# Optimization experiments

Measured on AMD Instinct MI355X. Metric: run time of the kernel, lower is better.

Reference implementation:

```python
import jax, jax.numpy as jnp
import numpy as np

N = 10000
E = 320000
D = 256   # hidden_dim
H = 4     # heads
C = D // H
NL = 3    # gat layers
EPS = 1e-5


def _ln(x, g, b):
    m = x.mean(-1, keepdims=True)
    v = ((x - m) ** 2).mean(-1, keepdims=True)
    return (x - m) / jnp.sqrt(v + EPS) * g + b


def setup_inputs() -> dict:
    key = jax.random.key(0)
    ks = iter(jax.random.split(key, 64))
    rn = lambda shape, s=0.05: jax.random.normal(next(ks), shape, dtype=jnp.float32) * s
    inp = dict(
        x=jax.random.normal(next(ks), (N, 10), dtype=jnp.float32),
        edge_index=jax.random.randint(next(ks), (2, E), 0, N),
        edge_attr=jax.random.uniform(next(ks), (E, 3), dtype=jnp.float32),
        agent_features=jax.random.normal(next(ks), (1, 10), dtype=jnp.float32),
        # node encoder
        enc_w=rn((10, D)), enc_b=jnp.zeros(D), enc_g=jnp.ones(D), enc_bt=jnp.zeros(D),
        # adaptive virtual node
        vn_base=jnp.zeros(D), vn_w1=rn((D, D)), vn_b1=jnp.zeros(D),
        vn_g=jnp.ones(D), vn_bt=jnp.zeros(D), vn_w2=rn((D, D)), vn_b2=jnp.zeros(D),
        # stacked GAT layer params
        gat_w=rn((NL, D, D)), att_src=rn((NL, H, C)), att_dst=rn((NL, H, C)),
        att_edge=rn((NL, H, C)), edge_w=rn((NL, 3, D)), gat_b=jnp.zeros((NL, D)),
        ln_g=jnp.ones((NL, D)), ln_b=jnp.zeros((NL, D)),
        # agent encoder
        ag_w=rn((10, D)), ag_b=jnp.zeros(D), ag_g=jnp.ones(D), ag_bt=jnp.zeros(D),
        # dueling heads (jk_dim = D*(NL+1) + D)
        v_w1=rn((D * (NL + 2), D)), v_b1=jnp.zeros(D), v_g=jnp.ones(D), v_bt=jnp.zeros(D),
        v_w2=rn((D, 1)), v_b2=jnp.zeros(1),
        a_w1=rn((D * (NL + 2), D)), a_b1=jnp.zeros(D), a_g=jnp.ones(D), a_bt=jnp.zeros(D),
        a_w2=rn((D, 9)), a_b2=jnp.zeros(9),
    )
    return inp


def _gat_layer(h, src, dst, eattr, lin_w, a_s, a_d, a_e, e_w, bias, n_seg):
    xs = (h @ lin_w).reshape(-1, H, C)                       # [Nt,H,C]
    al_s = (xs * a_s).sum(-1)                                # [Nt,H]
    al_d = (xs * a_d).sum(-1)
    ee = (eattr @ e_w).reshape(-1, H, C)                     # [Et,H,C]
    al_e = (ee * a_e).sum(-1)                                # [Et,H]
    alpha = jax.nn.leaky_relu(al_s[src] + al_d[dst] + al_e, 0.2)
    mx = jax.ops.segment_max(alpha, dst, num_segments=n_seg)
    a = jnp.exp(alpha - mx[dst])
    s = jax.ops.segment_sum(a, dst, num_segments=n_seg)
    a = a / (s[dst] + 1e-16)
    msg = xs[src] * a[:, :, None]                            # [Et,H,C]
    out = jax.ops.segment_sum(msg, dst, num_segments=n_seg)
    return out.reshape(n_seg, D) + bias


def reference(x, edge_index, edge_attr, agent_features,
              enc_w, enc_b, enc_g, enc_bt,
              vn_base, vn_w1, vn_b1, vn_g, vn_bt, vn_w2, vn_b2,
              gat_w, att_src, att_dst, att_edge, edge_w, gat_b, ln_g, ln_b,
              ag_w, ag_b, ag_g, ag_bt,
              v_w1, v_b1, v_g, v_bt, v_w2, v_b2,
              a_w1, a_b1, a_g, a_bt, a_w2, a_b2):
    n = x.shape[0]
    nt = n + 1  # + virtual node
    h0 = jax.nn.relu(_ln(x @ enc_w + enc_b, enc_g, enc_bt))
    ctx = h0.mean(0)
    ad = jnp.tanh(jax.nn.relu(_ln(ctx @ vn_w1 + vn_b1, vn_g, vn_bt)) @ vn_w2 + vn_b2)
    vn = vn_base + ad
    h = jnp.concatenate([h0, vn[None]], axis=0)              # [Nt,D]

    # virtual-node edges (bidirectional) with edge_attr = [0.5,0,0]
    ar = jnp.arange(n)
    vfull = jnp.full((n,), n, dtype=edge_index.dtype)
    src0 = jnp.concatenate([edge_index[0], vfull, ar])
    dst0 = jnp.concatenate([edge_index[1], ar, vfull])
    veattr = jnp.concatenate([jnp.full((2 * n, 1), 0.5), jnp.zeros((2 * n, 2))], axis=1)
    eattr0 = jnp.concatenate([edge_attr, veattr], axis=0)

    # GATConv add_self_loops with fill_value='mean' (mean of incoming edge_attr)
    deg = jax.ops.segment_sum(jnp.ones_like(dst0, dtype=jnp.float32), dst0, num_segments=nt)
    loop_attr = jax.ops.segment_sum(eattr0, dst0, num_segments=nt) / jnp.maximum(deg, 1.0)[:, None]
    loops = jnp.arange(nt, dtype=edge_index.dtype)
    src = jnp.concatenate([src0, loops])
    dst = jnp.concatenate([dst0, loops])
    eattr = jnp.concatenate([eattr0, loop_attr], axis=0)

    outs = [h]
    for i in range(NL):
        hn = _gat_layer(h, src, dst, eattr, gat_w[i], att_src[i], att_dst[i],
                        att_edge[i], edge_w[i], gat_b[i], nt)
        hn = _ln(hn, ln_g[i], ln_b[i])
        h = jax.nn.relu(hn + h)
        outs.append(h)
    jk = jnp.concatenate(outs, axis=-1)                      # [Nt, D*(NL+1)]

    global_repr = jk[-1][None]                               # virtual node row
    agent = jax.nn.relu(_ln(agent_features @ ag_w + ag_b, ag_g, ag_bt))
    comb = jnp.concatenate([global_repr, agent], axis=-1)
    val = jax.nn.relu(_ln(comb @ v_w1 + v_b1, v_g, v_bt)) @ v_w2 + v_b2
    adv = jax.nn.relu(_ln(comb @ a_w1 + a_b1, a_g, a_bt)) @ a_w2 + a_b2
    return val + (adv - adv.mean(axis=1, keepdims=True))
```

## Files before the change

kernel.cpp:

```cpp
#include <hip/hip_runtime.h>
#include <math.h>

#define NN 10000
#define EE 320000
#define DD 256
#define NT 10001
#define E1C (EE + NN)
#define E2C (EE + 2 * NN)
#define ETC (E2C + NT)
#define VB 157

typedef __attribute__((ext_vector_type(8))) short s16x8;
typedef __attribute__((ext_vector_type(4))) float f32x4;

__device__ __forceinline__ unsigned short f2bf(float f) {
    unsigned u = __float_as_uint(f);
    return (unsigned short)((u + 0x7FFFu + ((u >> 16) & 1u)) >> 16);
}
__device__ __forceinline__ float bf2f(unsigned short u) {
    return __uint_as_float((unsigned)u << 16);
}

__device__ __forceinline__ float wave_sum(float v) {
#pragma unroll
    for (int o = 32; o > 0; o >>= 1) v += __shfl_down(v, o, 64);
    return v;
}
__device__ __forceinline__ float blk_sum256(float v, float* sm4) {
    v = wave_sum(v);
    int lane = threadIdx.x & 63, w = threadIdx.x >> 6;
    __syncthreads();
    if (lane == 0) sm4[w] = v;
    __syncthreads();
    return sm4[0] + sm4[1] + sm4[2] + sm4[3];
}
__device__ __forceinline__ float2 blk_sum2(float a, float b, float2* sm4) {
#pragma unroll
    for (int o = 32; o > 0; o >>= 1) {
        a += __shfl_down(a, o, 64);
        b += __shfl_down(b, o, 64);
    }
    int lane = threadIdx.x & 63, w = threadIdx.x >> 6;
    __syncthreads();
    if (lane == 0) sm4[w] = make_float2(a, b);
    __syncthreads();
    float2 r;
    r.x = sm4[0].x + sm4[1].x + sm4[2].x + sm4[3].x;
    r.y = sm4[0].y + sm4[1].y + sm4[2].y + sm4[3].y;
    return r;
}

__global__ void __launch_bounds__(256) k_enc(
        const float* __restrict__ x, const float* __restrict__ wenc,
        const float* __restrict__ bia, const float* __restrict__ g,
        const float* __restrict__ bt, float* __restrict__ h,
        unsigned short* __restrict__ hb) {
    int t = threadIdx.x, lane = t & 63, wv = t >> 6;
    int v = blockIdx.x * 4 + wv;
    if (v >= NN) return;
    float xv = (lane < 10) ? x[v * 10 + lane] : 0.f;
    float4 acc = *(const float4*)(bia + lane * 4);
#pragma unroll
    for (int k = 0; k < 10; k++) {
        float xk = __shfl(xv, k, 64);
        float4 wk = *(const float4*)(wenc + k * DD + lane * 4);
        acc.x += xk * wk.x; acc.y += xk * wk.y; acc.z += xk * wk.z; acc.w += xk * wk.w;
    }
    float s1 = acc.x + acc.y + acc.z + acc.w;
    float s2 = acc.x * acc.x + acc.y * acc.y + acc.z * acc.z + acc.w * acc.w;
#pragma unroll
    for (int o = 32; o > 0; o >>= 1) {
        s1 += __shfl_xor(s1, o, 64);
        s2 += __shfl_xor(s2, o, 64);
    }
    float m = s1 * (1.f / DD);
    float var = s2 * (1.f / DD) - m * m;
    float rs = rsqrtf(var + 1e-5f);
    float4 g4 = *(const float4*)(g + lane * 4);
    float4 b4 = *(const float4*)(bt + lane * 4);
    float4 r4;
    r4.x = fmaxf((acc.x - m) * rs * g4.x + b4.x, 0.f);
    r4.y = fmaxf((acc.y - m) * rs * g4.y + b4.y, 0.f);
    r4.z = fmaxf((acc.z - m) * rs * g4.z + b4.z, 0.f);
    r4.w = fmaxf((acc.w - m) * rs * g4.w + b4.w, 0.f);
    *(float4*)(h + (size_t)v * DD + lane * 4) = r4;
    ushort4 u4;
    u4.x = f2bf(r4.x); u4.y = f2bf(r4.y); u4.z = f2bf(r4.z); u4.w = f2bf(r4.w);
    *(ushort4*)(hb + (size_t)v * DD + lane * 4) = u4;
}

__global__ void __launch_bounds__(256) k_ctx1deg(const float* __restrict__ h,
                                                 float* __restrict__ part,
                                                 const int* __restrict__ ei,
                                                 int* __restrict__ degi) {
    __shared__ float4 sm[4][64];
    int t = threadIdx.x, lane = t & 63, w = t >> 6;
    int b = blockIdx.x;
    float4 acc = make_float4(0.f, 0.f, 0.f, 0.f);
    for (int v = b * 4 + w; v < NN; v += 1024) {
        float4 hv = *(const float4*)(h + (size_t)v * DD + lane * 4);
        acc.x += hv.x; acc.y += hv.y; acc.z += hv.z; acc.w += hv.w;
    }
    sm[w][lane] = acc;
    __syncthreads();
    if (t < 64) {
        float4 a0 = sm[0][t], a1 = sm[1][t], a2 = sm[2][t], a3 = sm[3][t];
        float4 r;
        r.x = a0.x + a1.x + a2.x + a3.x;
        r.y = a0.y + a1.y + a2.y + a3.y;
        r.z = a0.z + a1.z + a2.z + a3.z;
        r.w = a0.w + a1.w + a2.w + a3.w;
        *(float4*)(part + (size_t)b * DD + t * 4) = r;
    }
    for (int e = b * 256 + t; e < EE; e += 256 * 256)
        atomicAdd(&degi[ei[EE + e]], 1);
}

__global__ void k_vn(const float* __restrict__ part,
                     const float* __restrict__ w1, const float* __restrict__ b1,
                     const float* __restrict__ g, const float* __restrict__ bt,
                     const float* __restrict__ w2, const float* __restrict__ b2,
                     const float* __restrict__ vnb,
                     float* __restrict__ h, unsigned short* __restrict__ hb,
                     float* __restrict__ comb) {
    __shared__ float2 sm4[4];
    __shared__ float cs[DD];
    __shared__ float t[DD];
    int j = threadIdx.x;
    float c = 0.f;
    for (int b = 0; b < 256; b++) c += part[(size_t)b * DD + j];
    cs[j] = c * (1.f / NN);
    __syncthreads();
    float acc = b1[j];
    for (int k = 0; k < DD; k++) acc += cs[k] * w1[k * DD + j];
    float2 mm = blk_sum2(acc, acc * acc, sm4);
    float m = mm.x * (1.f / DD);
    float var = mm.y * (1.f / DD) - m * m;
    float y = fmaxf((acc - m) * rsqrtf(var + 1e-5f) * g[j] + bt[j], 0.f);
    t[j] = y;
    __syncthreads();
    float a2 = b2[j];
    for (int k = 0; k < DD; k++) a2 += t[k] * w2[k * DD + j];
    float vn = vnb[j] + tanhf(a2);
    h[(size_t)NN * DD + j] = vn;
    hb[(size_t)NN * DD + j] = f2bf(vn);
    comb[j] = vn;
}

__global__ void k_scan(const int* __restrict__ degi, int* __restrict__ offs,
                       int* __restrict__ cursor) {
    __shared__ int wsum[16];
    __shared__ int running_s;
    int t = threadIdx.x, lane = t & 63, w = t >> 6;
    if (t == 0) running_s = 0;
    __syncthreads();
    for (int base = 0; base < NT; base += 1024) {
        int v = base + t;
        int val = 0;
        if (v < NN) val = degi[v] + 2;
        else if (v == NN) val = NN + 1;
        int x = val;
#pragma unroll
        for (int o = 1; o < 64; o <<= 1) {
            int y = __shfl_up(x, o, 64);
            if (lane >= o) x += y;
        }
        if (lane == 63) wsum[w] = x;
        __syncthreads();
        int prefix = running_s;
        for (int ww = 0; ww < w; ww++) prefix += wsum[ww];
        if (v <= NN) { int e0 = prefix + x - val; offs[v] = e0; cursor[v] = e0; }
        __syncthreads();
        if (t == 0) {
            int s = 0;
            for (int i = 0; i < 16; i++) s += wsum[i];
            running_s += s;
        }
        __syncthreads();
    }
    if (threadIdx.x == 0) offs[NT] = running_s;
}

__global__ void k_scatter(const int* __restrict__ ei, int* __restrict__ cursor,
                          int* __restrict__ ssrc, int* __restrict__ seid) {
    int e = blockIdx.x * 256 + threadIdx.x;
    if (e >= EE) return;
    int src = ei[e], dst = ei[EE + e];
    int pos = atomicAdd(&cursor[dst], 1);
    ssrc[pos] = src;
    seid[pos] = e;
}

__global__ void k_flattr(const int* __restrict__ offs, int* __restrict__ ssrc,
                         int* __restrict__ seid,
                         const float* __restrict__ ea, float* __restrict__ lattr) {
    int t = threadIdx.x, lane = t & 63, w = t >> 6;
    int v = blockIdx.x * 4 + w;
    if (v > NN) return;
    int bN = offs[NN];
    if (v == NN) {
        if (lane == 0) {
            lattr[v * 3] = 0.5f; lattr[v * 3 + 1] = 0.f; lattr[v * 3 + 2] = 0.f;
            ssrc[bN + NN] = NN; seid[bN + NN] = E2C + NN;
        }
        return;
    }
    int b0 = offs[v], e1 = offs[v + 1];
    if (lane == 0) {
        ssrc[e1 - 2] = NN; seid[e1 - 2] = EE + v;
        ssrc[e1 - 1] = v;  seid[e1 - 1] = E2C + v;
        ssrc[bN + v] = v;  seid[bN + v] = E1C + v;
    }
    int cnt = e1 - b0 - 2;
    float s0 = 0.f, s1 = 0.f, s2 = 0.f;
    for (int i = lane; i < cnt; i += 64) {
        int e = seid[b0 + i];
        s0 += ea[e * 3];
        s1 += ea[e * 3 + 1];
        s2 += ea[e * 3 + 2];
    }
    s0 = wave_sum(s0); s1 = wave_sum(s1); s2 = wave_sum(s2);
    if (lane == 0) {
        float inv = 1.f / (float)(cnt + 1);
        lattr[v * 3]     = (s0 + 0.5f) * inv;
        lattr[v * 3 + 1] = s1 * inv;
        lattr[v * 3 + 2] = s2 * inv;
    }
}

__global__ void k_wconv(const float* __restrict__ gw, unsigned short* __restrict__ wt,
                        const float* __restrict__ ew, const float* __restrict__ ae,
                        float* __restrict__ wd) {
    int b = blockIdx.x, j = threadIdx.x;
    if (b == 768) {
        if (j >= 36) return;
        int l = j / 12, k = (j / 4) % 3, h = j % 4;
        float s = 0.f;
        for (int c = 0; c < 64; c++)
            s += ew[l * 768 + k * DD + h * 64 + c] * ae[l * DD + h * 64 + c];
        wd[j] = s;
        return;
    }
    int l = b >> 8, k = b & 255;
    float v = gw[l * 65536 + k * 256 + j];
    wt[l * 65536 + j * 256 + k] = f2bf(v);
}

__global__ void k_edot(const int* __restrict__ seid, const float* __restrict__ ea,
                       const float* __restrict__ lattr, const float* __restrict__ wd,
                       unsigned short* __restrict__ edot) {
    int p = blockIdx.x * 256 + threadIdx.x;
    if (p >= ETC) return;
    int e = seid[p];
    float a0, a1, a2;
    if (e < EE)       { a0 = ea[e * 3]; a1 = ea[e * 3 + 1]; a2 = ea[e * 3 + 2]; }
    else if (e < E2C) { a0 = 0.5f; a1 = 0.f; a2 = 0.f; }
    else              { int v = e - E2C; a0 = lattr[v * 3]; a1 = lattr[v * 3 + 1]; a2 = lattr[v * 3 + 2]; }
#pragma unroll
    for (int l = 0; l < 3; l++) {
        ushort4 o;
        o.x = f2bf(a0 * wd[l * 12 + 0] + a1 * wd[l * 12 + 4] + a2 * wd[l * 12 + 8]);
        o.y = f2bf(a0 * wd[l * 12 + 1] + a1 * wd[l * 12 + 5] + a2 * wd[l * 12 + 9]);
        o.z = f2bf(a0 * wd[l * 12 + 2] + a1 * wd[l * 12 + 6] + a2 * wd[l * 12 + 10]);
        o.w = f2bf(a0 * wd[l * 12 + 3] + a1 * wd[l * 12 + 7] + a2 * wd[l * 12 + 11]);
        *(ushort4*)(edot + (size_t)l * ETC * 4 + (size_t)p * 4) = o;
    }
}

__global__ void __launch_bounds__(256) k_gemm_mfma(
        const unsigned short* __restrict__ hb, const unsigned short* __restrict__ wt,
        const float* __restrict__ as_, const float* __restrict__ ad_,
        unsigned short* __restrict__ xsb, float* __restrict__ als, float* __restrict__ ald) {
    __shared__ unsigned short tile[64][128];
    int bx = blockIdx.x;
    int v0 = (bx >> 1) * 64;
    int n0 = (bx & 1) * 128;
    int t = threadIdx.x, lane = t & 63, w = t >> 6;
    int rbase = v0 + w * 16;
    int li = lane & 15, g = lane >> 4;
    int arow = rbase + li; if (arow > NN) arow = NN;
    int koff = g * 8;
    const unsigned short* aptr = hb + (size_t)arow * DD + koff;
    const unsigned short* bptr = wt + (size_t)(n0 + li) * DD + koff;
    f32x4 acc[8];
#pragma unroll
    for (int n = 0; n < 8; n++) acc[n] = (f32x4){0.f, 0.f, 0.f, 0.f};
#pragma unroll
    for (int kb = 0; kb < 8; kb++) {
        s16x8 af = *(const s16x8*)(aptr + kb * 32);
#pragma unroll
        for (int n = 0; n < 8; n++) {
            s16x8 bf = *(const s16x8*)(bptr + (size_t)n * 16 * DD + kb * 32);
            acc[n] = __builtin_amdgcn_mfma_f32_16x16x32_bf16(af, bf, acc[n], 0, 0, 0);
        }
    }
    float asv[8], adv[8];
#pragma unroll
    for (int n = 0; n < 8; n++) { asv[n] = as_[n0 + n * 16 + li]; adv[n] = ad_[n0 + n * 16 + li]; }
    int hg0 = n0 >> 6;
#pragma unroll
    for (int r = 0; r < 4; r++) {
        int vrow = rbase + 4 * g + r;
#pragma unroll
        for (int h = 0; h < 2; h++) {
            float ps = acc[4 * h][r] * asv[4 * h] + acc[4 * h + 1][r] * asv[4 * h + 1]
                     + acc[4 * h + 2][r] * asv[4 * h + 2] + acc[4 * h + 3][r] * asv[4 * h + 3];
            float pd = acc[4 * h][r] * adv[4 * h] + acc[4 * h + 1][r] * adv[4 * h + 1]
                     + acc[4 * h + 2][r] * adv[4 * h + 2] + acc[4 * h + 3][r] * adv[4 * h + 3];
#pragma unroll
            for (int o = 1; o < 16; o <<= 1) {
                ps += __shfl_xor(ps, o, 64);
                pd += __shfl_xor(pd, o, 64);
            }
            if (li == 0 && vrow <= NN) { als[vrow * 4 + hg0 + h] = ps; ald[vrow * 4 + hg0 + h] = pd; }
        }
    }
#pragma unroll
    for (int n = 0; n < 8; n++)
#pragma unroll
        for (int r = 0; r < 4; r++)
            tile[w * 16 + 4 * g + r][n * 16 + li] = f2bf(acc[n][r]);
#pragma unroll
    for (int it = 0; it < 4; it++) {
        int flat = it * 64 + lane;
        int row = w * 16 + (flat >> 4);
        int c8 = flat & 15;
        int vrow = v0 + row;
        if (vrow <= NN)
            *(uint4*)(xsb + (size_t)vrow * DD + n0 + c8 * 8) = *(const uint4*)(&tile[row][c8 * 8]);
    }
}

__global__ void __launch_bounds__(256) k_msg(
        const int* __restrict__ offs, const int* __restrict__ ssrc,
        const unsigned short* __restrict__ edotL,
        const float* __restrict__ als, const float* __restrict__ ald,
        const unsigned short* __restrict__ xsb,
        const float* __restrict__ bias, const float* __restrict__ g,
        const float* __restrict__ bt, const float* __restrict__ hin,
        float* __restrict__ hout, unsigned short* __restrict__ hbout,
        float* __restrict__ pvacc, float* __restrict__ pws) {
    int v = blockIdx.x;
    if (v == NN) return;
    int t = threadIdx.x, lane = t & 63, w = t >> 6;
    int sub = lane >> 5, l32 = lane & 31, slot = w * 2 + sub;
    int hh = l32 >> 3;
    __shared__ float red[4][8][33];
    __shared__ float wsred[4][4];
    __shared__ float fin[4];
    __shared__ float2 sm4[4];
    float acc[8];
#pragma unroll
    for (int q = 0; q < 8; q++) acc[q] = 0.f;
    float swt = 0.f;
    if (v >= NT) {
        int b = v - NT;
        int b0 = offs[NN];
        float adh = ald[NN * 4 + hh];
        int i0 = b * 64, i1 = i0 + 64;
        if (i1 > NN + 1) i1 = NN + 1;
        for (int i = i0 + slot; i < i1; i += 8) {
            float a = als[i * 4 + hh] + bf2f(edotL[(size_t)(b0 + i) * 4 + hh]) + adh;
            a = a > 0.f ? a : 0.2f * a;
            float wt = __expf(a);
            uint4 xq = *(const uint4*)(xsb + (size_t)i * DD + l32 * 8);
            const unsigned short* xp = (const unsigned short*)&xq;
#pragma unroll
            for (int q = 0; q < 8; q++) acc[q] += wt * bf2f(xp[q]);
            if ((l32 & 7) == 0) swt += wt;
        }
#pragma unroll
        for (int q = 0; q < 8; q++) acc[q] += __shfl_xor(acc[q], 32, 64);
        swt += __shfl_xor(swt, 32, 64);
        if (sub == 0) {
#pragma unroll
            for (int q = 0; q < 8; q++) red[w][q][l32] = acc[q];
            if ((l32 & 7) == 0) wsred[w][hh] = swt;
        }
        __syncthreads();
        int c = t, q = c & 7, l = c >> 3;
        pvacc[(size_t)b * DD + c] = red[0][q][l] + red[1][q][l] + red[2][q][l] + red[3][q][l];
        if (t < 4) pws[b * 4 + t] = wsred[0][t] + wsred[1][t] + wsred[2][t] + wsred[3][t];
        return;
    }
    int b0 = offs[v], deg = offs[v + 1] - b0;
    float adh = ald[v * 4 + hh];
    for (int i = slot; i < deg; i += 8) {
        int p = b0 + i;
        int src = ssrc[p];
        float a = als[src * 4 + hh] + bf2f(edotL[(size_t)p * 4 + hh]) + adh;
        a = a > 0.f ? a : 0.2f * a;
        float wt = __expf(a);
        uint4 xq = *(const uint4*)(xsb + (size_t)src * DD + l32 * 8);
        const unsigned short* xp = (const unsigned short*)&xq;
#pragma unroll
        for (int q = 0; q < 8; q++) acc[q] += wt * bf2f(xp[q]);
        if ((l32 & 7) == 0) swt += wt;
    }
#pragma unroll
    for (int q = 0; q < 8; q++) acc[q] += __shfl_xor(acc[q], 32, 64);
    swt += __shfl_xor(swt, 32, 64);
    if (sub == 0) {
#pragma unroll
        for (int q = 0; q < 8; q++) red[w][q][l32] = acc[q];
        if ((l32 & 7) == 0) wsred[w][hh] = swt;
    }
    __syncthreads();
    if (t < 4) {
        float ws = wsred[0][t] + wsred[1][t] + wsred[2][t] + wsred[3][t];
        fin[t] = 1.f / (ws + 1e-16f);
    }
    __syncthreads();
    int c = t, q = c & 7, l = c >> 3;
    float o = (red[0][q][l] + red[1][q][l] + red[2][q][l] + red[3][q][l]) * fin[c >> 6];
    float tt = o + bias[c];
    float2 mm = blk_sum2(tt, tt * tt, sm4);
    float m = mm.x * (1.f / DD);
    float var = mm.y * (1.f / DD) - m * m;
    float y = (tt - m) * rsqrtf(var + 1e-5f) * g[c] + bt[c];
    float r = fmaxf(y + hin[(size_t)v * DD + c], 0.f);
    hout[(size_t)v * DD + c] = r;
    hbout[(size_t)v * DD + c] = f2bf(r);
}

__global__ void k_vpost(const float* __restrict__ pvacc, const float* __restrict__ pws,
                        const float* __restrict__ bias, const float* __restrict__ g,
                        const float* __restrict__ bt, const float* __restrict__ hin,
                        float* __restrict__ hout, unsigned short* __restrict__ hb,
                        float* __restrict__ jkslot,
                        int last, const float* __restrict__ af,
                        const float* __restrict__ agw, const float* __restrict__ agb,
                        const float* __restrict__ agg, const float* __restrict__ agbt,
                        float* __restrict__ comb) {
    __shared__ float2 sm4[4];
    int j = threadIdx.x, hh = j >> 6;
    float acc = 0.f;
    for (int b = 0; b < VB; b++) acc += pvacc[(size_t)b * DD + j];
    float ws = 0.f;
    for (int b = 0; b < VB; b++) ws += pws[b * 4 + hh];
    float o = acc / (ws + 1e-16f);
    float tt = o + bias[j];
    float2 mm = blk_sum2(tt, tt * tt, sm4);
    float m = mm.x * (1.f / DD);
    float var = mm.y * (1.f / DD) - m * m;
    float y = (tt - m) * rsqrtf(var + 1e-5f) * g[j] + bt[j];
    float r = fmaxf(y + hin[(size_t)NN * DD + j], 0.f);
    hout[(size_t)NN * DD + j] = r;
    hb[(size_t)NN * DD + j] = f2bf(r);
    jkslot[j] = r;
    if (last) {
        float a2 = agb[j];
#pragma unroll
        for (int k = 0; k < 10; k++) a2 += af[k] * agw[k * DD + j];
        float2 m2 = blk_sum2(a2, a2 * a2, sm4);
        float mu = m2.x * (1.f / DD);
        float vv = m2.y * (1.f / DD) - mu * mu;
        float ya = (a2 - mu) * rsqrtf(vv + 1e-5f) * agg[j] + agbt[j];
        comb[1024 + j] = fmaxf(ya, 0.f);
    }
}

__global__ void k_head(const float* __restrict__ comb,
                       const float* __restrict__ vw1, const float* __restrict__ aw1,
                       float* __restrict__ pv, float* __restrict__ pa,
                       int* __restrict__ cnt,
                       const float* __restrict__ vb1, const float* __restrict__ vg,
                       const float* __restrict__ vbt, const float* __restrict__ vw2,
                       const float* __restrict__ vb2,
                       const float* __restrict__ ab1, const float* __restrict__ ag,
                       const float* __restrict__ abt, const float* __restrict__ aw2,
                       const float* __restrict__ ab2, float* __restrict__ out) {
    __shared__ float2 sm4[4];
    __shared__ float sm1[4];
    __shared__ float tl[DD];
    __shared__ float adv[9];
    __shared__ float valv;
    __shared__ int islast;
    int j = threadIdx.x, s = blockIdx.x;
    int k0 = s * 32;
    float accv = 0.f, acca = 0.f;
#pragma unroll
    for (int kk = 0; kk < 32; kk++) {
        float c = comb[k0 + kk];
        accv += c * vw1[(k0 + kk) * DD + j];
        acca += c * aw1[(k0 + kk) * DD + j];
    }
    pv[s * DD + j] = accv;
    pa[s * DD + j] = acca;
    __threadfence();
    if (j == 0) islast = (atomicAdd(cnt, 1) == 39) ? 1 : 0;
    __syncthreads();
    if (!islast) return;
    __threadfence();
    float acc = vb1[j], acc2 = ab1[j];
    for (int ss = 0; ss < 40; ss++) { acc += pv[ss * DD + j]; acc2 += pa[ss * DD + j]; }
    float2 mm = blk_sum2(acc, acc * acc, sm4);
    float m = mm.x * (1.f / DD);
    float var = mm.y * (1.f / DD) - m * m;
    float y = fmaxf((acc - m) * rsqrtf(var + 1e-5f) * vg[j] + vbt[j], 0.f);
    float vs = blk_sum256(y * vw2[j], sm1);
    if (j == 0) valv = vs + vb2[0];
    float2 mm2 = blk_sum2(acc2, acc2 * acc2, sm4);
    float m2 = mm2.x * (1.f / DD);
    float var2 = mm2.y * (1.f / DD) - m2 * m2;
    float y2 = fmaxf((acc2 - m2) * rsqrtf(var2 + 1e-5f) * ag[j] + abt[j], 0.f);
    tl[j] = y2;
    __syncthreads();
    if (j < 9) {
        float ss = ab2[j];
        for (int k = 0; k < DD; k++) ss += tl[k] * aw2[k * 9 + j];
        adv[j] = ss;
    }
    __syncthreads();
    if (j < 9) {
        float mean = 0.f;
        for (int o = 0; o < 9; o++) mean += adv[o];
        mean *= (1.f / 9.f);
        out[j] = valv + adv[j] - mean;
    }
}

extern "C" void kernel_launch(void* const* d_in, const int* in_sizes, int n_in,
                              void* d_out, int out_size, void* d_ws, size_t ws_size,
                              hipStream_t stream) {
    (void)in_sizes; (void)n_in; (void)out_size; (void)ws_size;
    const float* x      = (const float*)d_in[0];
    const int*   ei     = (const int*)d_in[1];
    const float* ea     = (const float*)d_in[2];
    const float* af     = (const float*)d_in[3];
    const float* enc_w  = (const float*)d_in[4];
    const float* enc_b  = (const float*)d_in[5];
    const float* enc_g  = (const float*)d_in[6];
    const float* enc_bt = (const float*)d_in[7];
    const float* vn_base= (const float*)d_in[8];
    const float* vn_w1  = (const float*)d_in[9];
    const float* vn_b1  = (const float*)d_in[10];
    const float* vn_g   = (const float*)d_in[11];
    const float* vn_bt  = (const float*)d_in[12];
    const float* vn_w2  = (const float*)d_in[13];
    const float* vn_b2  = (const float*)d_in[14];
    const float* gat_w  = (const float*)d_in[15];
    const float* att_src= (const float*)d_in[16];
    const float* att_dst= (const float*)d_in[17];
    const float* att_edge=(const float*)d_in[18];
    const float* edge_w = (const float*)d_in[19];
    const float* gat_b  = (const float*)d_in[20];
    const float* ln_g   = (const float*)d_in[21];
    const float* ln_b   = (const float*)d_in[22];
    const float* ag_w   = (const float*)d_in[23];
    const float* ag_b   = (const float*)d_in[24];
    const float* ag_g   = (const float*)d_in[25];
    const float* ag_bt  = (const float*)d_in[26];
    const float* v_w1   = (const float*)d_in[27];
    const float* v_b1   = (const float*)d_in[28];
    const float* v_g    = (const float*)d_in[29];
    const float* v_bt   = (const float*)d_in[30];
    const float* v_w2   = (const float*)d_in[31];
    const float* v_b2   = (const float*)d_in[32];
    const float* a_w1   = (const float*)d_in[33];
    const float* a_b1   = (const float*)d_in[34];
    const float* a_g    = (const float*)d_in[35];
    const float* a_bt   = (const float*)d_in[36];
    const float* a_w2   = (const float*)d_in[37];
    const float* a_b2   = (const float*)d_in[38];

    char* p = (char*)d_ws;
    auto alloc = [&](size_t bytes) {
        char* r = p;
        p += (bytes + 255) & ~(size_t)255;
        return r;
    };
    float* big0  = (float*)alloc((size_t)NT * DD * 4);
    float* big2  = (float*)alloc((size_t)NT * DD * 4);
    unsigned short* hb   = (unsigned short*)alloc((size_t)NT * DD * 2);
    unsigned short* xsb  = (unsigned short*)alloc((size_t)NT * DD * 2);
    unsigned short* wt   = (unsigned short*)alloc((size_t)3 * DD * DD * 2);
    unsigned short* edot = (unsigned short*)alloc((size_t)3 * ETC * 4 * 2);
    int* ssrc    = (int*)alloc((size_t)ETC * 4);
    int* seid    = (int*)alloc((size_t)ETC * 4);
    float* als   = (float*)alloc((size_t)NT * 4 * 4);
    float* ald   = (float*)alloc((size_t)NT * 4 * 4);
    float* part  = (float*)alloc((size_t)256 * DD * 4);
    float* comb  = (float*)alloc(1280 * 4);
    float* lattr = (float*)alloc((size_t)NT * 3 * 4);
    float* wd    = (float*)alloc(36 * 4);
    float* pvacc = (float*)alloc((size_t)VB * DD * 4);
    float* pws   = (float*)alloc((size_t)VB * 4 * 4);
    float* pv    = (float*)alloc(40 * DD * 4);
    float* pa    = (float*)alloc(40 * DD * 4);
    int* degi    = (int*)alloc((size_t)(NT + 16) * 4);
    int* cnt     = degi + NT;
    int* offs    = (int*)alloc((size_t)(NT + 1) * 4);
    int* cursor  = (int*)alloc((size_t)NT * 4);

    hipMemsetAsync(degi, 0, (size_t)(NT + 16) * 4, stream);

    k_enc<<<2500, 256, 0, stream>>>(x, enc_w, enc_b, enc_g, enc_bt, big0, hb);
    k_ctx1deg<<<256, 256, 0, stream>>>(big0, part, ei, degi);
    k_vn<<<1, 256, 0, stream>>>(part, vn_w1, vn_b1, vn_g, vn_bt, vn_w2, vn_b2, vn_base, big0, hb, comb);
    k_scan<<<1, 1024, 0, stream>>>(degi, offs, cursor);
    k_scatter<<<(EE + 255) / 256, 256, 0, stream>>>(ei, cursor, ssrc, seid);
    k_flattr<<<(NT + 3) / 4, 256, 0, stream>>>(offs, ssrc, seid, ea, lattr);
    k_wconv<<<769, 256, 0, stream>>>(gat_w, wt, edge_w, att_edge, wd);
    k_edot<<<(ETC + 255) / 256, 256, 0, stream>>>(seid, ea, lattr, wd, edot);

    float* cur = big0;
    float* po  = big2;
    for (int l = 0; l < 3; l++) {
        const unsigned short* edotL = edot + (size_t)l * ETC * 4;
        k_gemm_mfma<<<((NT + 63) / 64) * 2, 256, 0, stream>>>(hb, wt + (size_t)l * DD * DD,
                                                              att_src + l * DD, att_dst + l * DD,
                                                              xsb, als, ald);
        k_msg<<<NT + VB, 256, 0, stream>>>(offs, ssrc, edotL, als, ald, xsb,
                                           gat_b + l * DD, ln_g + l * DD, ln_b + l * DD,
                                           cur, po, hb, pvacc, pws);
        k_vpost<<<1, 256, 0, stream>>>(pvacc, pws, gat_b + l * DD, ln_g + l * DD, ln_b + l * DD,
                                       cur, po, hb, comb + (l + 1) * DD,
                                       (l == 2) ? 1 : 0, af, ag_w, ag_b, ag_g, ag_bt, comb);
        float* t = cur; cur = po; po = t;
    }
    k_head<<<40, 256, 0, stream>>>(comb, v_w1, a_w1, pv, pa, cnt,
                                   v_b1, v_g, v_bt, v_w2, v_b2,
                                   a_b1, a_g, a_bt, a_w2, a_b2, (float*)d_out);
}
```

Measured before the change: 368.3 us.

## Process one destination node per wavefront in GAT message kernel

The message/aggregation kernel now assigns one wavefront per destination node, with four nodes per block, instead of one 256-thread block per node. Each wave first computes the attention weights for up to 64 edges in parallel, with one lane per edge, and stages them with the source ids in shared memory. It then loops over those edges with each lane accumulating 4 channels, and does the LayerNorm with wave shuffles instead of block-level shared-memory reductions and syncthreads. This removes cross-wave reductions and barriers and cuts the block count, but the gather loop over edges is now serial within one wave, so the memory-level parallelism per node is lower.

```diff
diff --git a/kernel.cpp b/kernel.cpp
--- a/kernel.cpp
+++ b/kernel.cpp
@@ -9,6 +9,7 @@
 #define E2C (EE + 2 * NN)
 #define ETC (E2C + NT)
 #define VB 157
+#define RB 2500
 
 typedef __attribute__((ext_vector_type(8))) short s16x8;
 typedef __attribute__((ext_vector_type(4))) float f32x4;
@@ -340,25 +341,22 @@
         const float* __restrict__ bt, const float* __restrict__ hin,
         float* __restrict__ hout, unsigned short* __restrict__ hbout,
         float* __restrict__ pvacc, float* __restrict__ pws) {
-    int v = blockIdx.x;
-    if (v == NN) return;
+    int b = blockIdx.x;
     int t = threadIdx.x, lane = t & 63, w = t >> 6;
-    int sub = lane >> 5, l32 = lane & 31, slot = w * 2 + sub;
-    int hh = l32 >> 3;
-    __shared__ float red[4][8][33];
-    __shared__ float wsred[4][4];
-    __shared__ float fin[4];
-    __shared__ float2 sm4[4];
-    float acc[8];
-#pragma unroll
-    for (int q = 0; q < 8; q++) acc[q] = 0.f;
-    float swt = 0.f;
-    if (v >= NT) {
-        int b = v - NT;
+    if (b >= RB) {
+        int sub = lane >> 5, l32 = lane & 31, slot = w * 2 + sub;
+        int hh = l32 >> 3;
+        __shared__ float red[4][8][33];
+        __shared__ float wsred[4][4];
+        int bb = b - RB;
         int b0 = offs[NN];
         float adh = ald[NN * 4 + hh];
-        int i0 = b * 64, i1 = i0 + 64;
+        int i0 = bb * 64, i1 = i0 + 64;
         if (i1 > NN + 1) i1 = NN + 1;
+        float acc[8];
+#pragma unroll
+        for (int q = 0; q < 8; q++) acc[q] = 0.f;
+        float swt = 0.f;
         for (int i = i0 + slot; i < i1; i += 8) {
             float a = als[i * 4 + hh] + bf2f(edotL[(size_t)(b0 + i) * 4 + hh]) + adh;
             a = a > 0.f ? a : 0.2f * a;
@@ -379,48 +377,74 @@
         }
         __syncthreads();
         int c = t, q = c & 7, l = c >> 3;
-        pvacc[(size_t)b * DD + c] = red[0][q][l] + red[1][q][l] + red[2][q][l] + red[3][q][l];
-        if (t < 4) pws[b * 4 + t] = wsred[0][t] + wsred[1][t] + wsred[2][t] + wsred[3][t];
+        pvacc[(size_t)bb * DD + c] = red[0][q][l] + red[1][q][l] + red[2][q][l] + red[3][q][l];
+        if (t < 4) pws[bb * 4 + t] = wsred[0][t] + wsred[1][t] + wsred[2][t] + wsred[3][t];
         return;
     }
+    __shared__ int   lsrc[4][64];
+    __shared__ float lw[4][64][4];
+    int v = b * 4 + w;
     int b0 = offs[v], deg = offs[v + 1] - b0;
-    float adh = ald[v * 4 + hh];
-    for (int i = slot; i < deg; i += 8) {
-        int p = b0 + i;
-        int src = ssrc[p];
-        float a = als[src * 4 + hh] + bf2f(edotL[(size_t)p * 4 + hh]) + adh;
-        a = a > 0.f ? a : 0.2f * a;
-        float wt = __expf(a);
-        uint4 xq = *(const uint4*)(xsb + (size_t)src * DD + l32 * 8);
-        const unsigned short* xp = (const unsigned short*)&xq;
-#pragma unroll
-        for (int q = 0; q < 8; q++) acc[q] += wt * bf2f(xp[q]);
-        if ((l32 & 7) == 0) swt += wt;
-    }
-#pragma unroll
-    for (int q = 0; q < 8; q++) acc[q] += __shfl_xor(acc[q], 32, 64);
-    swt += __shfl_xor(swt, 32, 64);
-    if (sub == 0) {
-#pragma unroll
-        for (int q = 0; q < 8; q++) red[w][q][l32] = acc[q];
-        if ((l32 & 7) == 0) wsred[w][hh] = swt;
-    }
-    __syncthreads();
-    if (t < 4) {
-        float ws = wsred[0][t] + wsred[1][t] + wsred[2][t] + wsred[3][t];
-        fin[t] = 1.f / (ws + 1e-16f);
-    }
-    __syncthreads();
-    int c = t, q = c & 7, l = c >> 3;
-    float o = (red[0][q][l] + red[1][q][l] + red[2][q][l] + red[3][q][l]) * fin[c >> 6];
-    float tt = o + bias[c];
-    float2 mm = blk_sum2(tt, tt * tt, sm4);
-    float m = mm.x * (1.f / DD);
-    float var = mm.y * (1.f / DD) - m * m;
-    float y = (tt - m) * rsqrtf(var + 1e-5f) * g[c] + bt[c];
-    float r = fmaxf(y + hin[(size_t)v * DD + c], 0.f);
-    hout[(size_t)v * DD + c] = r;
-    hbout[(size_t)v * DD + c] = f2bf(r);
+    int hh = lane >> 4;
+    float4 ad4 = *(const float4*)(ald + v * 4);
+    float a0c = 0.f, a1c = 0.f, a2c = 0.f, a3c = 0.f;
+    float ws = 0.f;
+    for (int base = 0; base < deg; base += 64) {
+        int rem = deg - base; if (rem > 64) rem = 64;
+        if (lane < rem) {
+            int p = b0 + base + lane;
+            int src = ssrc[p];
+            lsrc[w][lane] = src;
+            ushort4 ed = *(const ushort4*)(edotL + (size_t)p * 4);
+            float4 a4 = *(const float4*)(als + src * 4);
+            float f0 = a4.x + bf2f(ed.x) + ad4.x; f0 = f0 > 0.f ? f0 : 0.2f * f0;
+            float f1 = a4.y + bf2f(ed.y) + ad4.y; f1 = f1 > 0.f ? f1 : 0.2f * f1;
+            float f2 = a4.z + bf2f(ed.z) + ad4.z; f2 = f2 > 0.f ? f2 : 0.2f * f2;
+            float f3 = a4.w + bf2f(ed.w) + ad4.w; f3 = f3 > 0.f ? f3 : 0.2f * f3;
+            lw[w][lane][0] = __expf(f0);
+            lw[w][lane][1] = __expf(f1);
+            lw[w][lane][2] = __expf(f2);
+            lw[w][lane][3] = __expf(f3);
+        }
+        for (int i = 0; i < rem; i++) {
+            float wt = lw[w][i][hh];
+            int src = lsrc[w][i];
+            ushort4 xq = *(const ushort4*)(xsb + (size_t)src * DD + lane * 4);
+            a0c += wt * bf2f(xq.x);
+            a1c += wt * bf2f(xq.y);
+            a2c += wt * bf2f(xq.z);
+            a3c += wt * bf2f(xq.w);
+            ws += wt;
+        }
+    }
+    float inv = 1.f / (ws + 1e-16f);
+    float4 bi4 = *(const float4*)(bias + lane * 4);
+    float t0 = a0c * inv + bi4.x;
+    float t1 = a1c * inv + bi4.y;
+    float t2 = a2c * inv + bi4.z;
+    float t3 = a3c * inv + bi4.w;
+    float s1 = t0 + t1 + t2 + t3;
+    float s2 = t0 * t0 + t1 * t1 + t2 * t2 + t3 * t3;
+#pragma unroll
+    for (int o = 32; o > 0; o >>= 1) {
+        s1 += __shfl_xor(s1, o, 64);
+        s2 += __shfl_xor(s2, o, 64);
+    }
+    float m = s1 * (1.f / DD);
+    float var = s2 * (1.f / DD) - m * m;
+    float rs = rsqrtf(var + 1e-5f);
+    float4 g4 = *(const float4*)(g + lane * 4);
+    float4 b4 = *(const float4*)(bt + lane * 4);
+    float4 h4 = *(const float4*)(hin + (size_t)v * DD + lane * 4);
+    float4 r4;
+    r4.x = fmaxf((t0 - m) * rs * g4.x + b4.x + h4.x, 0.f);
+    r4.y = fmaxf((t1 - m) * rs * g4.y + b4.y + h4.y, 0.f);
+    r4.z = fmaxf((t2 - m) * rs * g4.z + b4.z + h4.z, 0.f);
+    r4.w = fmaxf((t3 - m) * rs * g4.w + b4.w + h4.w, 0.f);
+    *(float4*)(hout + (size_t)v * DD + lane * 4) = r4;
+    ushort4 u4;
+    u4.x = f2bf(r4.x); u4.y = f2bf(r4.y); u4.z = f2bf(r4.z); u4.w = f2bf(r4.w);
+    *(ushort4*)(hbout + (size_t)v * DD + lane * 4) = u4;
 }
 
 __global__ void k_vpost(const float* __restrict__ pvacc, const float* __restrict__ pws,
@@ -611,7 +635,7 @@
         k_gemm_mfma<<<((NT + 63) / 64) * 2, 256, 0, stream>>>(hb, wt + (size_t)l * DD * DD,
                                                               att_src + l * DD, att_dst + l * DD,
                                                               xsb, als, ald);
-        k_msg<<<NT + VB, 256, 0, stream>>>(offs, ssrc, edotL, als, ald, xsb,
+        k_msg<<<RB + VB, 256, 0, stream>>>(offs, ssrc, edotL, als, ald, xsb,
                                            gat_b + l * DD, ln_g + l * DD, ln_b + l * DD,
                                            cur, po, hb, pvacc, pws);
         k_vpost<<<1, 256, 0, stream>>>(pvacc, pws, gat_b + l * DD, ln_g + l * DD, ln_b + l * DD,
```

After: 336.3 us (median of 2 runs). 1.1x faster.
